# Kernel tuning notes

Hardware: AMD Instinct MI355X
Metric: run time of the kernel (lower is better)

The kernel has to match this reference:

```python
import jax, jax.numpy as jnp
import numpy as np
import math

B, S, D, H, DFF = 16, 1024, 512, 8, 2048
DH = D // H
EPS = 1e-5


def setup_inputs() -> dict:
    key = jax.random.key(0)
    ks = jax.random.split(key, 16)
    sc = 0.02
    inp = {
        "x": jax.random.normal(ks[0], (B, S, D), dtype=jnp.float32),
        "mask": jnp.zeros((B, 1, 1, S), dtype=jnp.float32),
        # attention projections (stored as [in, out])
        "wq": jax.random.normal(ks[1], (D, D), jnp.float32) * sc,
        "bq": jnp.zeros((D,), jnp.float32),
        "wk": jax.random.normal(ks[2], (D, D), jnp.float32) * sc,
        "bk": jnp.zeros((D,), jnp.float32),
        "wv": jax.random.normal(ks[3], (D, D), jnp.float32) * sc,
        "bv": jnp.zeros((D,), jnp.float32),
        "wo": jax.random.normal(ks[4], (D, D), jnp.float32) * sc,
        "bo": jnp.zeros((D,), jnp.float32),
        # FFN
        "w1": jax.random.normal(ks[5], (D, DFF), jnp.float32) * sc,
        "b1": jnp.zeros((DFF,), jnp.float32),
        "w2": jax.random.normal(ks[6], (DFF, D), jnp.float32) * sc,
        "b2": jnp.zeros((D,), jnp.float32),
        # LayerNorms over the full [S, D] slab (normalized_shape=[S, D])
        "ln1_w": jnp.ones((S, D), jnp.float32),
        "ln1_b": jnp.zeros((S, D), jnp.float32),
        "ln2_w": jnp.ones((S, D), jnp.float32),
        "ln2_b": jnp.zeros((S, D), jnp.float32),
    }
    return inp


def _layernorm_2d(x, w, b):
    # torch nn.LayerNorm([S, D]): normalize jointly over last two dims
    m = jnp.mean(x, axis=(-2, -1), keepdims=True)
    v = jnp.mean(jnp.square(x - m), axis=(-2, -1), keepdims=True)
    return (x - m) * jax.lax.rsqrt(v + EPS) * w + b


def _encoder_layer(x, mask, wq, bq, wk, bk, wv, bv, wo, bo,
                   w1, b1, w2, b2, ln1_w, ln1_b, ln2_w, ln2_b):
    # --- multi-head attention ---
    def heads(t):  # [B,S,D] -> [B,H,S,DH]
        return t.reshape(B, S, H, DH).transpose(0, 2, 1, 3)

    q = heads(x @ wq + bq)
    k = heads(x @ wk + bk)
    v = heads(x @ wv + bv)

    logits = jnp.einsum("bhqd,bhkd->bhqk", q, k) / math.sqrt(DH)
    logits = logits + mask * -1e9
    attn = jax.nn.softmax(logits, axis=-1)          # [B,H,S,S]
    ctx = jnp.einsum("bhqk,bhkd->bhqd", attn, v)    # [B,H,S,DH]
    ctx = ctx.transpose(0, 2, 1, 3).reshape(B, S, D)
    attn_out = ctx @ wo + bo

    out1 = _layernorm_2d(x + attn_out, ln1_w, ln1_b)

    # --- FFN ---
    ffn = jax.nn.relu(out1 @ w1 + b1) @ w2 + b2
    out2 = _layernorm_2d(out1 + ffn, ln2_w, ln2_b)
    return out2


def reference(x, mask, wq, bq, wk, bk, wv, bv, wo, bo,
              w1, b1, w2, b2, ln1_w, ln1_b, ln2_w, ln2_b):
    return _encoder_layer(x, mask, wq, bq, wk, bk, wv, bv, wo, bo,
                          w1, b1, w2, b2, ln1_w, ln1_b, ln2_w, ln2_b)
```

## Files before the change

### kernel.cpp

```cpp
#include <hip/hip_runtime.h>
#include <stdint.h>

#define B_   16
#define S_   1024
#define D_   512
#define H_   8
#define DH_  64
#define DFF_ 2048
#define M_   (B_*S_)
#define SD_  (S_*D_)

typedef unsigned short u16;
typedef unsigned int u32;
typedef __attribute__((ext_vector_type(4))) unsigned short u16x4;
typedef __attribute__((ext_vector_type(8))) short bf16x8;
typedef __attribute__((ext_vector_type(4))) float f32x4;
typedef __attribute__((ext_vector_type(16))) float f32x16;

#define LOG2E 1.4426950408889634f

__device__ __forceinline__ u16 f2bf(float f) {
  union { float f; uint32_t u; } x{f};
  uint32_t r = x.u + 0x7fffu + ((x.u >> 16) & 1u);
  return (u16)(r >> 16);
}

__device__ __forceinline__ float bf2f(u16 v) {
  union { uint32_t u; float f; } x{(uint32_t)v << 16};
  return x.f;
}

__device__ __forceinline__ u32 pk2(float lo, float hi) {
  union { float f; u32 u; } a{lo}, b{hi};
  return __builtin_amdgcn_perm(b.u, a.u, 0x07060302u);
}

__device__ __forceinline__ float exp2fast(float x) {
#if __has_builtin(__builtin_amdgcn_exp2f)
  return __builtin_amdgcn_exp2f(x);
#else
  return exp2f(x);
#endif
}

__device__ __forceinline__ void gload16(const u16* g, u16* l) {
  __builtin_amdgcn_global_load_lds(
      (const __attribute__((address_space(1))) uint32_t*)g,
      (__attribute__((address_space(3))) uint32_t*)l, 16, 0, 0);
}

__device__ __forceinline__ int swz3(int r) { return (r & 7) ^ ((r >> 3) & 7); }

__global__ __launch_bounds__(256) void cast_x_kernel(const float* __restrict__ x,
                                                     u16* __restrict__ xb) {
  int i = blockIdx.x * 256 + threadIdx.x;
  f32x4 v = ((const f32x4*)x)[i];
  u16x4 o = { f2bf(v[0]), f2bf(v[1]), f2bf(v[2]), f2bf(v[3]) };
  ((u16x4*)xb)[i] = o;
}

__global__ __launch_bounds__(256) void transpose_cast_kernel(
    const float* __restrict__ W, u16* __restrict__ WT, int K, int N) {
  __shared__ float t[32][33];
  int n0 = blockIdx.x * 32, k0 = blockIdx.y * 32;
  int tx = threadIdx.x, ty = threadIdx.y;
  #pragma unroll
  for (int i = 0; i < 4; i++)
    t[ty + 8*i][tx] = W[(size_t)(k0 + ty + 8*i) * N + n0 + tx];
  __syncthreads();
  #pragma unroll
  for (int i = 0; i < 4; i++)
    WT[(size_t)(n0 + ty + 8*i) * K + k0 + tx] = f2bf(t[tx][ty + 8*i]);
}

template<int MODE, bool RELU>
__global__ __launch_bounds__(512, 2) void gemm256_kernel(
    const u16* __restrict__ A, const u16* __restrict__ WT,
    const float* __restrict__ bias0, const float* __restrict__ bias1,
    const float* __restrict__ bias2,
    u16* __restrict__ out0, u16* __restrict__ out1, u16* __restrict__ out2,
    int K, int ostride, int nx, int ypg) {
  __shared__ u16 lA[2][16384];
  __shared__ u16 lB[2][16384];
  int tid = threadIdx.x, lane = tid & 63;
  int wid = tid >> 6, wm = wid >> 2, wn = wid & 3;
  int l16 = lane & 15, kg4 = lane >> 4;

  int d = blockIdx.x;
  int c = d & 7, j = d >> 3;
  int x = j % nx, y = c * ypg + j / nx;
  int m0 = y * 256, n0 = x * 256;

  const u16* agp = A  + (size_t)m0 * K;
  const u16* bgp = WT + (size_t)n0 * K;
  int srow = tid >> 3, sslot = tid & 7;

  f32x4 z = {0.f, 0.f, 0.f, 0.f};
  f32x4 acc[8][4];
  #pragma unroll
  for (int mg = 0; mg < 8; mg++)
    #pragma unroll
    for (int ni = 0; ni < 4; ni++) acc[mg][ni] = z;

#define STAGE256(buf, kt) do { \
    _Pragma("unroll") \
    for (int h = 0; h < 2; h++) \
      _Pragma("unroll") \
      for (int i = 0; i < 2; i++) { \
        int r_ = h*128 + i*64 + srow; \
        int gc_ = (kt) + ((sslot ^ swz3(r_)) << 3); \
        gload16(agp + (size_t)r_ * K + gc_, &lA[buf][h*8192 + (i*512 + tid)*8]); \
        gload16(bgp + (size_t)r_ * K + gc_, &lB[buf][h*8192 + (i*512 + tid)*8]); \
      } \
  } while (0)

  int nk = K / 64;
  int cur = 0;
  STAGE256(0, 0);
  asm volatile("s_waitcnt vmcnt(0)" ::: "memory");
  __builtin_amdgcn_s_barrier();

  for (int t = 0; t < nk; t++) {
    if (t + 1 < nk) STAGE256(cur ^ 1, (t + 1) * 64);
    bf16x8 bfv[4][2];
    #pragma unroll
    for (int ni = 0; ni < 4; ni++)
      #pragma unroll
      for (int kf = 0; kf < 2; kf++) {
        int row = wn*64 + ni*16 + l16;
        int slot = (kf*4 + kg4) ^ swz3(row);
        bfv[ni][kf] = *(const bf16x8*)&lB[cur][row*64 + slot*8];
      }
    #pragma unroll
    for (int p = 0; p < 4; p++) {
      bf16x8 af[2][2];
      #pragma unroll
      for (int mi = 0; mi < 2; mi++)
        #pragma unroll
        for (int kf = 0; kf < 2; kf++) {
          int row = wm*128 + p*32 + mi*16 + l16;
          int slot = (kf*4 + kg4) ^ swz3(row);
          af[mi][kf] = *(const bf16x8*)&lA[cur][row*64 + slot*8];
        }
      __builtin_amdgcn_s_setprio(1);
      #pragma unroll
      for (int kf = 0; kf < 2; kf++)
        #pragma unroll
        for (int mi = 0; mi < 2; mi++)
          #pragma unroll
          for (int ni = 0; ni < 4; ni++)
            acc[p*2 + mi][ni] = __builtin_amdgcn_mfma_f32_16x16x32_bf16(
                af[mi][kf], bfv[ni][kf], acc[p*2 + mi][ni], 0, 0, 0);
      __builtin_amdgcn_s_setprio(0);
      __builtin_amdgcn_s_barrier();
      __builtin_amdgcn_sched_barrier(0);
    }
    asm volatile("s_waitcnt vmcnt(0)" ::: "memory");
    __builtin_amdgcn_s_barrier();
    cur ^= 1;
  }
#undef STAGE256

  int segbase = n0 + wn*64;
  int seg = segbase >> 9;
  const float* bp = (MODE == 2) ? (seg == 0 ? bias0 : (seg == 1 ? bias1 : bias2)) : bias0;
  u16* op = (MODE == 2) ? (seg == 0 ? out0 : (seg == 1 ? out1 : out2)) : out0;
  float aeff = (MODE == 2 && seg == 0) ? 0.125f * LOG2E : 1.0f;

  #pragma unroll
  for (int mg = 0; mg < 8; mg++)
    #pragma unroll
    for (int ni = 0; ni < 4; ni++) {
      int col = segbase + ni*16 + l16;
      int ocol = (MODE == 2) ? (col & 511) : col;
      float bv = bp[ocol];
      #pragma unroll
      for (int r = 0; r < 4; r++) {
        int row = m0 + wm*128 + mg*16 + kg4*4 + r;
        float v = (acc[mg][ni][r] + bv) * aeff;
        if (RELU) v = fmaxf(v, 0.f);
        op[(size_t)row * ostride + ocol] = f2bf(v);
      }
    }
}

template<int MODE, bool RELU, bool RESB>
__global__ __launch_bounds__(256) void gemm_kernel(
    const u16* __restrict__ A, const u16* __restrict__ WT,
    const float* __restrict__ bias0, const float* __restrict__ res,
    const u16* __restrict__ resB,
    u16* __restrict__ out0, float* __restrict__ outF,
    float* __restrict__ partOut, int K, int N, int nx, int ypg) {
  __shared__ u16 lA[2][128 * 32];
  __shared__ u16 lB[2][128 * 32];
  __shared__ float lred[8];
  int tid = threadIdx.x;
  int lane = tid & 63, wid = tid >> 6;
  int wr = wid >> 1, wc = wid & 1;
  int lrow = lane & 15, kg = lane >> 4;

  int dd = blockIdx.x;
  int cc = dd & 7, jj = dd >> 3;
  int bx = jj % nx, by = cc * ypg + jj / nx;
  int m0 = by * 128, n0 = bx * 128;

  int r0 = tid >> 2, c0 = (tid & 3) * 8;
  const u16* agp = A  + (size_t)m0 * K;
  const u16* bgp = WT + (size_t)n0 * K;

  f32x4 z = {0.f, 0.f, 0.f, 0.f};
  f32x4 acc[4][4];
  #pragma unroll
  for (int mi = 0; mi < 4; mi++)
    #pragma unroll
    for (int ni = 0; ni < 4; ni++) acc[mi][ni] = z;

#define STAGE_G(buf, kt) do { \
    gload16(agp + (size_t)r0 * K + (kt) + c0,        &lA[buf][tid * 8]); \
    gload16(agp + (size_t)(r0 + 64) * K + (kt) + c0, &lA[buf][2048 + tid * 8]); \
    gload16(bgp + (size_t)r0 * K + (kt) + c0,        &lB[buf][tid * 8]); \
    gload16(bgp + (size_t)(r0 + 64) * K + (kt) + c0, &lB[buf][2048 + tid * 8]); \
  } while (0)

  STAGE_G(0, 0);

  int nk = K / 32;
  int cur = 0;
  for (int t = 0; t < nk; t++) {
    if (t + 1 < nk) {
      STAGE_G(cur ^ 1, (t + 1) * 32);
      asm volatile("s_waitcnt vmcnt(4)" ::: "memory");
    } else {
      asm volatile("s_waitcnt vmcnt(0)" ::: "memory");
    }
    __syncthreads();
    bf16x8 af[4], bfv[4];
    #pragma unroll
    for (int mi = 0; mi < 4; mi++)
      af[mi] = *(const bf16x8*)&lA[cur][(wr*64 + mi*16 + lrow) * 32 + kg*8];
    #pragma unroll
    for (int ni = 0; ni < 4; ni++)
      bfv[ni] = *(const bf16x8*)&lB[cur][(wc*64 + ni*16 + lrow) * 32 + kg*8];
    #pragma unroll
    for (int mi = 0; mi < 4; mi++)
      #pragma unroll
      for (int ni = 0; ni < 4; ni++)
        acc[mi][ni] = __builtin_amdgcn_mfma_f32_16x16x32_bf16(af[mi], bfv[ni], acc[mi][ni], 0, 0, 0);
    __syncthreads();
    cur ^= 1;
  }
#undef STAGE_G

  float s_acc = 0.f, q_acc = 0.f;
  #pragma unroll
  for (int mi = 0; mi < 4; mi++)
    #pragma unroll
    for (int ni = 0; ni < 4; ni++) {
      int col = n0 + wc*64 + ni*16 + lrow;
      float bv = bias0[col];
      #pragma unroll
      for (int r = 0; r < 4; r++) {
        int row = m0 + wr*64 + mi*16 + kg*4 + r;
        float v = acc[mi][ni][r] + bv;
        if (RELU) v = fmaxf(v, 0.f);
        if (MODE == 1) {
          size_t off = (size_t)row * N + col;
          float rv = RESB ? bf2f(resB[off]) : res[off];
          float tv = v + rv;
          outF[off] = tv;
          s_acc += tv;
          q_acc += tv * tv;
        } else {
          out0[(size_t)row * N + col] = f2bf(v);
        }
      }
    }

  if (MODE == 1) {
    #pragma unroll
    for (int dsh = 1; dsh < 64; dsh <<= 1) {
      s_acc += __shfl_xor(s_acc, dsh);
      q_acc += __shfl_xor(q_acc, dsh);
    }
    if (lane == 0) { lred[wid*2] = s_acc; lred[wid*2+1] = q_acc; }
    __syncthreads();
    if (tid == 0) {
      int batch = by >> 3;
      int pidx = batch*32 + (by & 7)*nx + bx;
      partOut[pidx*2]   = lred[0]+lred[2]+lred[4]+lred[6];
      partOut[pidx*2+1] = lred[1]+lred[3]+lred[5]+lred[7];
    }
  }
}

__global__ __launch_bounds__(256) void attn_kernel(
    const u16* __restrict__ Q, const u16* __restrict__ Km,
    const u16* __restrict__ Vm, const float* __restrict__ mask,
    u16* __restrict__ ctx) {
  __shared__ u16 lK[2][4096];
  __shared__ u16 lV[2][4096];
  __shared__ float lBias[1024];
  int tid = threadIdx.x, lane = tid & 63, wid = tid >> 6;
  int la = lane & 31, hi = lane >> 5;
  int wg = blockIdx.x;
  int xcd = wg & 7, idx = wg >> 3;
  int bh = xcd * 16 + (idx & 15);
  int qt = idx >> 4;
  int b = bh >> 3, h = bh & 7;

  const u16* qp = Q + (size_t)(b*S_ + qt*128 + wid*32 + la) * D_ + h*DH_ + hi*8;
  bf16x8 qf[4];
  #pragma unroll
  for (int c = 0; c < 4; c++) qf[c] = *(const bf16x8*)(qp + c*16);

  int krow = tid >> 3;
  int kcol = 8 * (tid & 7);
  int kc0 = kcol ^ (swz3(krow) << 3);
  int kc1 = kcol ^ (swz3(krow + 32) << 3);
  int va = tid & 7, vp = tid >> 3;
  const u16* kbase = Km + ((size_t)b*S_) * D_ + h*DH_;
  const u16* vbase = Vm + ((size_t)b*S_) * D_ + h*DH_ + 8*va;

#define STAGE_K(buf, tt) do { \
    const u16* kt_ = kbase + (size_t)(tt)*64*D_; \
    gload16(kt_ + (size_t)krow*D_ + kc0,        &lK[buf][tid*8]); \
    gload16(kt_ + (size_t)(krow+32)*D_ + kc1,   &lK[buf][2048 + tid*8]); \
  } while (0)
#define LOAD_V(tt) do { \
    const u16* vt_ = vbase + (size_t)((tt)*64 + 2*vp) * D_; \
    nv0 = *(const bf16x8*)vt_; nv1 = *(const bf16x8*)(vt_ + D_); \
  } while (0)
#define WRITE_V(buf) do { \
    u32* lVd_ = (u32*)lV[buf]; \
    _Pragma("unroll") \
    for (int jv = 0; jv < 8; jv++) { \
      int row_ = 8*va + jv; \
      u32 pv_ = (u32)(u16)nv0[jv] | ((u32)(u16)nv1[jv] << 16); \
      lVd_[row_*32 + (vp ^ (swz3(row_) << 2))] = pv_; \
    } \
  } while (0)

  {
    f32x4 mv = ((const f32x4*)(mask + (size_t)b*S_))[tid];
    f32x4 bv;
    #pragma unroll
    for (int jj = 0; jj < 4; jj++) bv[jj] = mv[jj] * (-1.0e9f * LOG2E);
    ((f32x4*)lBias)[tid] = bv;
  }

  bf16x8 nv0, nv1;
  STAGE_K(0, 0);
  LOAD_V(0);
  WRITE_V(0);
  __syncthreads();

  f32x16 oc0, oc1;
  #pragma unroll
  for (int i = 0; i < 16; i++) { oc0[i] = 0.f; oc1[i] = 0.f; }
  float lsum = 0.f;
  int cur = 0;
  int swk0 = swz3(la) << 2, swk1 = swz3(la + 32) << 2;

  for (int t = 0; t < S_/64; t++) {
    if (t + 1 < S_/64) { STAGE_K(cur ^ 1, t + 1); LOAD_V(t + 1); }

    f32x16 s0, s1;
    #pragma unroll
    for (int rq = 0; rq < 4; rq++) {
      f32x4 bb0 = *(const f32x4*)&lBias[t*64 + rq*8 + hi*4];
      f32x4 bb1 = *(const f32x4*)&lBias[t*64 + 32 + rq*8 + hi*4];
      #pragma unroll
      for (int jj = 0; jj < 4; jj++) { s0[rq*4+jj] = bb0[jj]; s1[rq*4+jj] = bb1[jj]; }
    }
    __builtin_amdgcn_s_setprio(1);
    #pragma unroll
    for (int c = 0; c < 4; c++) {
      int dwb = c*8 + hi*4;
      bf16x8 kf0 = *(const bf16x8*)&lK[cur][la*64 + ((dwb ^ swk0) << 1)];
      bf16x8 kf1 = *(const bf16x8*)&lK[cur][(la+32)*64 + ((dwb ^ swk1) << 1)];
      s0 = __builtin_amdgcn_mfma_f32_32x32x16_bf16(kf0, qf[c], s0, 0, 0, 0);
      s1 = __builtin_amdgcn_mfma_f32_32x32x16_bf16(kf1, qf[c], s1, 0, 0, 0);
    }
    __builtin_amdgcn_s_setprio(0);
    float rs = 0.f;
    #pragma unroll
    for (int i = 0; i < 16; i++) { float e = exp2fast(s0[i]); s0[i] = e; rs += e; }
    #pragma unroll
    for (int i = 0; i < 16; i++) { float e = exp2fast(s1[i]); s1[i] = e; rs += e; }
    lsum += rs;
    __builtin_amdgcn_s_setprio(1);
    #pragma unroll
    for (int cc = 0; cc < 4; cc++) {
      const int base = 8 * (cc & 1);
      float pv[8];
      #pragma unroll
      for (int k = 0; k < 8; k++) pv[k] = (cc < 2) ? s0[base + k] : s1[base + k];
      u32 a0 = pk2(pv[0], pv[1]);
      u32 a1 = pk2(pv[2], pv[3]);
      u32 b0 = pk2(pv[4], pv[5]);
      u32 b1 = pk2(pv[6], pv[7]);
      u32 sd0 = hi ? a0 : b0, sd1 = hi ? a1 : b1;
      u32 x0 = (u32)__shfl_xor((int)sd0, 32);
      u32 x1 = (u32)__shfl_xor((int)sd1, 32);
      union { u32 u[4]; bf16x8 v; } pf;
      pf.u[0] = hi ? x0 : a0;
      pf.u[1] = hi ? x1 : a1;
      pf.u[2] = hi ? b0 : x0;
      pf.u[3] = hi ? b1 : x1;
      #pragma unroll
      for (int vb = 0; vb < 2; vb++) {
        int row = vb*32 + la;
        int dwv = (cc*8 + hi*4) ^ (swz3(row) << 2);
        bf16x8 vf = *(const bf16x8*)&lV[cur][row*64 + (dwv << 1)];
        if (vb == 0) oc0 = __builtin_amdgcn_mfma_f32_32x32x16_bf16(pf.v, vf, oc0, 0, 0, 0);
        else         oc1 = __builtin_amdgcn_mfma_f32_32x32x16_bf16(pf.v, vf, oc1, 0, 0, 0);
      }
    }
    __builtin_amdgcn_s_setprio(0);
    if (t + 1 < S_/64) {
      WRITE_V(cur ^ 1);
      __syncthreads();
      cur ^= 1;
    }
  }
#undef STAGE_K
#undef LOAD_V
#undef WRITE_V
  lsum += __shfl_xor(lsum, 32);
  float linv = 1.f / lsum;
  #pragma unroll
  for (int r = 0; r < 16; r++) {
    int qr = (r&3) + 8*(r>>2) + 4*hi;
    float lr = __shfl(linv, qr);
    size_t rowoff = (size_t)(b*S_ + qt*128 + wid*32 + qr) * D_ + h*DH_;
    ctx[rowoff + la]      = f2bf(oc0[r] * lr);
    ctx[rowoff + 32 + la] = f2bf(oc1[r] * lr);
  }
}

template<bool WB, bool WF>
__global__ __launch_bounds__(256) void ln_apply_kernel(
    const float* __restrict__ r, const float* __restrict__ part,
    const float* __restrict__ w, const float* __restrict__ bb,
    float* __restrict__ outF, u16* __restrict__ outB) {
  int b = blockIdx.y, c = blockIdx.x, tid = threadIdx.x;
  float s = 0.f, q = 0.f;
  for (int i = 0; i < 32; i++) { s += part[(b*32+i)*2]; q += part[(b*32+i)*2+1]; }
  const float inv = 1.f / (float)SD_;
  float mean = s * inv;
  float var = q * inv - mean * mean;
  float rs = rsqrtf(var + 1e-5f);
  size_t base = (size_t)b * SD_;
  #pragma unroll
  for (int i = 0; i < 8; i++) {
    int li4 = c*2048 + i*256 + tid;
    f32x4 v  = ((const f32x4*)(r + base))[li4];
    f32x4 wv = ((const f32x4*)w)[li4];
    f32x4 bv = ((const f32x4*)bb)[li4];
    f32x4 ov;
    #pragma unroll
    for (int jj = 0; jj < 4; jj++) ov[jj] = (v[jj] - mean) * rs * wv[jj] + bv[jj];
    if (WF) ((f32x4*)(outF + base))[li4] = ov;
    if (WB) {
      u16x4 ub = { f2bf(ov[0]), f2bf(ov[1]), f2bf(ov[2]), f2bf(ov[3]) };
      ((u16x4*)(outB + base))[li4] = ub;
    }
  }
}

extern "C" void kernel_launch(void* const* d_in, const int* in_sizes, int n_in,
                              void* d_out, int out_size, void* d_ws, size_t ws_size,
                              hipStream_t stream) {
  (void)in_sizes; (void)n_in; (void)out_size; (void)ws_size;
  const float* x    = (const float*)d_in[0];
  const float* mask = (const float*)d_in[1];
  const float* wq = (const float*)d_in[2];
  const float* bq = (const float*)d_in[3];
  const float* wk = (const float*)d_in[4];
  const float* bk = (const float*)d_in[5];
  const float* wv = (const float*)d_in[6];
  const float* bv = (const float*)d_in[7];
  const float* wo = (const float*)d_in[8];
  const float* bo = (const float*)d_in[9];
  const float* w1 = (const float*)d_in[10];
  const float* b1 = (const float*)d_in[11];
  const float* w2 = (const float*)d_in[12];
  const float* b2 = (const float*)d_in[13];
  const float* ln1w = (const float*)d_in[14];
  const float* ln1b = (const float*)d_in[15];
  const float* ln2w = (const float*)d_in[16];
  const float* ln2b = (const float*)d_in[17];
  float* out = (float*)d_out;

  char* ws = (char*)d_ws;
  const size_t MB = 1ull << 20;
  u16*   xb    = (u16*)(ws + 0);
  u16*   Qb    = (u16*)(ws + 16*MB);
  u16*   Kb    = (u16*)(ws + 32*MB);
  u16*   Vb    = (u16*)(ws + 48*MB);
  u16*   ctxb  = (u16*)(ws + 64*MB);
  float* res1  = (float*)(ws + 80*MB);
  u16*   out1b = (u16*)(ws + 0);
  u16*   ffn1  = (u16*)(ws + 16*MB);
  float* res2  = (float*)(ws + 112*MB);
  float* part  = (float*)(ws + 144*MB);
  u16*   wqkvT = (u16*)(ws + 145*MB);
  u16*   woT   = (u16*)(ws + 147*MB);
  u16*   w1T   = (u16*)(ws + 148*MB);
  u16*   w2T   = (u16*)(ws + 150*MB);

  dim3 tb(32, 8);
  cast_x_kernel<<<8192, 256, 0, stream>>>(x, xb);
  transpose_cast_kernel<<<dim3(16,16), tb, 0, stream>>>(wq, wqkvT,            512, 512);
  transpose_cast_kernel<<<dim3(16,16), tb, 0, stream>>>(wk, wqkvT + 512*512,  512, 512);
  transpose_cast_kernel<<<dim3(16,16), tb, 0, stream>>>(wv, wqkvT + 1024*512, 512, 512);
  transpose_cast_kernel<<<dim3(16,16), tb, 0, stream>>>(wo, woT, 512, 512);
  transpose_cast_kernel<<<dim3(64,16), tb, 0, stream>>>(w1, w1T, 512, 2048);
  transpose_cast_kernel<<<dim3(16,64), tb, 0, stream>>>(w2, w2T, 2048, 512);

  gemm256_kernel<2,false><<<384, 512, 0, stream>>>(
      xb, wqkvT, bq, bk, bv, Qb, Kb, Vb, 512, 512, 6, 8);

  attn_kernel<<<1024, 256, 0, stream>>>(Qb, Kb, Vb, mask, ctxb);

  gemm_kernel<1,false,false><<<512, 256, 0, stream>>>(
      ctxb, woT, bo, x, nullptr, nullptr, res1, part, 512, 512, 4, 16);

  ln_apply_kernel<true,false><<<dim3(64,16), 256, 0, stream>>>(
      res1, part, ln1w, ln1b, nullptr, out1b);

  gemm256_kernel<0,true><<<512, 512, 0, stream>>>(
      out1b, w1T, b1, nullptr, nullptr, ffn1, nullptr, nullptr, 512, 2048, 8, 8);

  gemm_kernel<1,false,true><<<512, 256, 0, stream>>>(
      ffn1, w2T, b2, nullptr, out1b, nullptr, res2, part, 2048, 512, 4, 16);

  ln_apply_kernel<false,true><<<dim3(64,16), 256, 0, stream>>>(
      res2, part, ln2w, ln2b, out, nullptr);
}
```

Before: 268.4 us.

## Store residuals in bf16, simplify GEMM syncs, skip zero attention-mask bias

The projection and FFN-down GEMM epilogues now write the residual sum as bf16 instead of fp32, and the LayerNorm apply kernel reads bf16. This halves the residual write and read traffic, at the cost of extra rounding before normalization. Both GEMM kernels restructure their synchronization to one __syncthreads per k-step and drop the per-subtile barriers in the 256 kernel; the 128 kernel also raises wave priority around its MFMA block. The attention kernel checks at runtime whether the mask is all zeros and, if so, skips loading the bias from LDS.

```diff
diff --git a/kernel.cpp b/kernel.cpp
--- a/kernel.cpp
+++ b/kernel.cpp
@@ -117,10 +117,9 @@
   int nk = K / 64;
   int cur = 0;
   STAGE256(0, 0);
-  asm volatile("s_waitcnt vmcnt(0)" ::: "memory");
-  __builtin_amdgcn_s_barrier();
 
   for (int t = 0; t < nk; t++) {
+    __syncthreads();
     if (t + 1 < nk) STAGE256(cur ^ 1, (t + 1) * 64);
     bf16x8 bfv[4][2];
     #pragma unroll
@@ -152,11 +151,8 @@
             acc[p*2 + mi][ni] = __builtin_amdgcn_mfma_f32_16x16x32_bf16(
                 af[mi][kf], bfv[ni][kf], acc[p*2 + mi][ni], 0, 0, 0);
       __builtin_amdgcn_s_setprio(0);
-      __builtin_amdgcn_s_barrier();
       __builtin_amdgcn_sched_barrier(0);
     }
-    asm volatile("s_waitcnt vmcnt(0)" ::: "memory");
-    __builtin_amdgcn_s_barrier();
     cur ^= 1;
   }
 #undef STAGE256
@@ -189,7 +185,7 @@
     const u16* __restrict__ A, const u16* __restrict__ WT,
     const float* __restrict__ bias0, const float* __restrict__ res,
     const u16* __restrict__ resB,
-    u16* __restrict__ out0, float* __restrict__ outF,
+    u16* __restrict__ out0,
     float* __restrict__ partOut, int K, int N, int nx, int ypg) {
   __shared__ u16 lA[2][128 * 32];
   __shared__ u16 lB[2][128 * 32];
@@ -227,13 +223,8 @@
   int nk = K / 32;
   int cur = 0;
   for (int t = 0; t < nk; t++) {
-    if (t + 1 < nk) {
-      STAGE_G(cur ^ 1, (t + 1) * 32);
-      asm volatile("s_waitcnt vmcnt(4)" ::: "memory");
-    } else {
-      asm volatile("s_waitcnt vmcnt(0)" ::: "memory");
-    }
     __syncthreads();
+    if (t + 1 < nk) STAGE_G(cur ^ 1, (t + 1) * 32);
     bf16x8 af[4], bfv[4];
     #pragma unroll
     for (int mi = 0; mi < 4; mi++)
@@ -241,12 +232,13 @@
     #pragma unroll
     for (int ni = 0; ni < 4; ni++)
       bfv[ni] = *(const bf16x8*)&lB[cur][(wc*64 + ni*16 + lrow) * 32 + kg*8];
+    __builtin_amdgcn_s_setprio(1);
     #pragma unroll
     for (int mi = 0; mi < 4; mi++)
       #pragma unroll
       for (int ni = 0; ni < 4; ni++)
         acc[mi][ni] = __builtin_amdgcn_mfma_f32_16x16x32_bf16(af[mi], bfv[ni], acc[mi][ni], 0, 0, 0);
-    __syncthreads();
+    __builtin_amdgcn_s_setprio(0);
     cur ^= 1;
   }
 #undef STAGE_G
@@ -263,15 +255,15 @@
         int row = m0 + wr*64 + mi*16 + kg*4 + r;
         float v = acc[mi][ni][r] + bv;
         if (RELU) v = fmaxf(v, 0.f);
+        size_t off = (size_t)row * N + col;
         if (MODE == 1) {
-          size_t off = (size_t)row * N + col;
           float rv = RESB ? bf2f(resB[off]) : res[off];
           float tv = v + rv;
-          outF[off] = tv;
+          out0[off] = f2bf(tv);
           s_acc += tv;
           q_acc += tv * tv;
         } else {
-          out0[(size_t)row * N + col] = f2bf(v);
+          out0[off] = f2bf(v);
         }
       }
     }
@@ -300,6 +292,7 @@
   __shared__ u16 lK[2][4096];
   __shared__ u16 lV[2][4096];
   __shared__ float lBias[1024];
+  __shared__ int lFlag[4];
   int tid = threadIdx.x, lane = tid & 63, wid = tid >> 6;
   int la = lane & 31, hi = lane >> 5;
   int wg = blockIdx.x;
@@ -342,6 +335,9 @@
 
   {
     f32x4 mv = ((const f32x4*)(mask + (size_t)b*S_))[tid];
+    bool zl = (mv[0] == 0.f) & (mv[1] == 0.f) & (mv[2] == 0.f) & (mv[3] == 0.f);
+    int wz = __all(zl) ? 1 : 0;
+    if (lane == 0) lFlag[wid] = wz;
     f32x4 bv;
     #pragma unroll
     for (int jj = 0; jj < 4; jj++) bv[jj] = mv[jj] * (-1.0e9f * LOG2E);
@@ -353,6 +349,7 @@
   LOAD_V(0);
   WRITE_V(0);
   __syncthreads();
+  const bool skip_bias = (lFlag[0] & lFlag[1] & lFlag[2] & lFlag[3]) != 0;
 
   f32x16 oc0, oc1;
   #pragma unroll
@@ -365,12 +362,17 @@
     if (t + 1 < S_/64) { STAGE_K(cur ^ 1, t + 1); LOAD_V(t + 1); }
 
     f32x16 s0, s1;
-    #pragma unroll
-    for (int rq = 0; rq < 4; rq++) {
-      f32x4 bb0 = *(const f32x4*)&lBias[t*64 + rq*8 + hi*4];
-      f32x4 bb1 = *(const f32x4*)&lBias[t*64 + 32 + rq*8 + hi*4];
-      #pragma unroll
-      for (int jj = 0; jj < 4; jj++) { s0[rq*4+jj] = bb0[jj]; s1[rq*4+jj] = bb1[jj]; }
+    if (skip_bias) {
+      #pragma unroll
+      for (int i = 0; i < 16; i++) { s0[i] = 0.f; s1[i] = 0.f; }
+    } else {
+      #pragma unroll
+      for (int rq = 0; rq < 4; rq++) {
+        f32x4 bb0 = *(const f32x4*)&lBias[t*64 + rq*8 + hi*4];
+        f32x4 bb1 = *(const f32x4*)&lBias[t*64 + 32 + rq*8 + hi*4];
+        #pragma unroll
+        for (int jj = 0; jj < 4; jj++) { s0[rq*4+jj] = bb0[jj]; s1[rq*4+jj] = bb1[jj]; }
+      }
     }
     __builtin_amdgcn_s_setprio(1);
     #pragma unroll
@@ -440,7 +442,7 @@
 
 template<bool WB, bool WF>
 __global__ __launch_bounds__(256) void ln_apply_kernel(
-    const float* __restrict__ r, const float* __restrict__ part,
+    const u16* __restrict__ r, const float* __restrict__ part,
     const float* __restrict__ w, const float* __restrict__ bb,
     float* __restrict__ outF, u16* __restrict__ outB) {
   int b = blockIdx.y, c = blockIdx.x, tid = threadIdx.x;
@@ -454,12 +456,12 @@
   #pragma unroll
   for (int i = 0; i < 8; i++) {
     int li4 = c*2048 + i*256 + tid;
-    f32x4 v  = ((const f32x4*)(r + base))[li4];
+    u16x4 rv = ((const u16x4*)(r + base))[li4];
     f32x4 wv = ((const f32x4*)w)[li4];
     f32x4 bv = ((const f32x4*)bb)[li4];
     f32x4 ov;
     #pragma unroll
-    for (int jj = 0; jj < 4; jj++) ov[jj] = (v[jj] - mean) * rs * wv[jj] + bv[jj];
+    for (int jj = 0; jj < 4; jj++) ov[jj] = (bf2f(rv[jj]) - mean) * rs * wv[jj] + bv[jj];
     if (WF) ((f32x4*)(outF + base))[li4] = ov;
     if (WB) {
       u16x4 ub = { f2bf(ov[0]), f2bf(ov[1]), f2bf(ov[2]), f2bf(ov[3]) };
@@ -499,10 +501,10 @@
   u16*   Kb    = (u16*)(ws + 32*MB);
   u16*   Vb    = (u16*)(ws + 48*MB);
   u16*   ctxb  = (u16*)(ws + 64*MB);
-  float* res1  = (float*)(ws + 80*MB);
+  u16*   res1b = (u16*)(ws + 80*MB);
   u16*   out1b = (u16*)(ws + 0);
   u16*   ffn1  = (u16*)(ws + 16*MB);
-  float* res2  = (float*)(ws + 112*MB);
+  u16*   res2b = (u16*)(ws + 112*MB);
   float* part  = (float*)(ws + 144*MB);
   u16*   wqkvT = (u16*)(ws + 145*MB);
   u16*   woT   = (u16*)(ws + 147*MB);
@@ -524,17 +526,17 @@
   attn_kernel<<<1024, 256, 0, stream>>>(Qb, Kb, Vb, mask, ctxb);
 
   gemm_kernel<1,false,false><<<512, 256, 0, stream>>>(
-      ctxb, woT, bo, x, nullptr, nullptr, res1, part, 512, 512, 4, 16);
+      ctxb, woT, bo, x, nullptr, res1b, part, 512, 512, 4, 16);
 
   ln_apply_kernel<true,false><<<dim3(64,16), 256, 0, stream>>>(
-      res1, part, ln1w, ln1b, nullptr, out1b);
+      res1b, part, ln1w, ln1b, nullptr, out1b);
 
   gemm256_kernel<0,true><<<512, 512, 0, stream>>>(
       out1b, w1T, b1, nullptr, nullptr, ffn1, nullptr, nullptr, 512, 2048, 8, 8);
 
   gemm_kernel<1,false,true><<<512, 256, 0, stream>>>(
-      ffn1, w2T, b2, nullptr, out1b, nullptr, res2, part, 2048, 512, 4, 16);
+      ffn1, w2T, b2, nullptr, out1b, res2b, part, 2048, 512, 4, 16);
 
   ln_apply_kernel<false,true><<<dim3(64,16), 256, 0, stream>>>(
-      res2, part, ln2w, ln2b, out, nullptr);
-}
+      res2b, part, ln2w, ln2b, out, nullptr);
+}
```

After: 259.8 us. 1.03x faster.
